# Optimization experiments

Measured on AMD Instinct MI355X. Metric: run time of the kernel, lower is better.

## Reference

```python
import jax, jax.numpy as jnp
import numpy as np

RADIUS = 0.07          # gno_config.gno_radius
SCALES = (1.0, 2.0)    # gno_config.scales


def _kernel_mlp(pair, kW1, kb1, kW2, kb2, kW3, kb3):
    # ChannelMLP inside IntegralTransform: gelu between layers, none after last
    h = jax.nn.gelu(pair @ kW1 + kb1)
    h = jax.nn.gelu(h @ kW2 + kb2)
    return h @ kW3 + kb3


def setup_inputs() -> dict:
    key = jax.random.key(0)
    ks = jax.random.split(key, 8)
    B, N, NL, CD, IN_C, C, H = 2, 2048, 512, 2, 16, 32, 32

    def glorot(k, shape):
        return jax.random.normal(k, shape) / jnp.sqrt(jnp.float32(shape[0]))

    return {
        "x_coord": jax.random.uniform(ks[0], (B, N, CD), dtype=jnp.float32),
        "pndata": jax.random.normal(ks[1], (B, N, IN_C), dtype=jnp.float32),
        "latent_tokens_coord": jax.random.uniform(ks[2], (NL, CD), dtype=jnp.float32),
        # lifting ChannelMLP (n_layers=1 -> single 1x1 conv == linear)
        "W_lift": glorot(ks[3], (IN_C, C)),
        "b_lift": jnp.zeros((C,), jnp.float32),
        # kernel MLP: [2*coord_dim=4] -> 32 -> 32 -> out_channels=32
        "kW1": glorot(ks[4], (2 * CD, H)),
        "kb1": jnp.zeros((H,), jnp.float32),
        "kW2": glorot(ks[5], (H, H)),
        "kb2": jnp.zeros((H,), jnp.float32),
        "kW3": glorot(ks[6], (H, C)),
        "kb3": jnp.zeros((C,), jnp.float32),
    }


def reference(x_coord, pndata, latent_tokens_coord,
              W_lift, b_lift, kW1, kb1, kW2, kb2, kW3, kb3):
    # lifting: [B,N,in_c] -> [B,N,C]
    f = pndata @ W_lift + b_lift

    B, N, CD = x_coord.shape
    NL = latent_tokens_coord.shape[0]

    y = x_coord[:, None, :, :]                      # [B,1,N,CD] source coords
    xq = latent_tokens_coord[None, :, None, :]      # [1,NL,1,CD] query coords
    # kernel input = cat(y_j, x_i) per (query i, source j) pair -> [B,NL,N,2*CD]
    pair = jnp.concatenate([jnp.broadcast_to(y, (B, NL, N, CD)),
                            jnp.broadcast_to(xq, (B, NL, N, CD))], axis=-1)
    kvals = _kernel_mlp(pair, kW1, kb1, kW2, kb2, kW3, kb3)  # [B,NL,N,C]

    d2 = jnp.sum((y - xq) ** 2, axis=-1)            # [B,NL,N] squared distances

    out = jnp.zeros((B, NL, kvals.shape[-1]), f.dtype)
    for s in SCALES:  # fixed small set of scales (2)
        # radius neighbor search expressed as dense mask (faithful to ball query)
        mask = (d2 <= (RADIUS * s) ** 2).astype(f.dtype)      # [B,NL,N]
        cnt = jnp.maximum(jnp.sum(mask, axis=-1), 1.0)        # [B,NL]
        # 'linear' transform: mean_j k(x_i,y_j) * f(y_j) over neighbors
        agg = jnp.einsum('bijc,bjc,bij->bic', kvals, f, mask)
        out = out + agg / cnt[..., None]
    return out  # [B,NL,C]
```

## Files before the change

kernel.cpp:

```cpp
#include <hip/hip_runtime.h>

static constexpr int B_ = 2, N_ = 2048, NL_ = 512, IN_C_ = 16, C_ = 32, H_ = 32;
static constexpr float R1SQ = (float)(0.07 * 0.07);
static constexpr float R2SQ = (float)(0.14 * 0.14);

typedef __attribute__((ext_vector_type(8))) short bf16x8;
typedef __attribute__((ext_vector_type(4))) float f32x4;

__device__ __forceinline__ float gelu_tanh(float x) {
    float z2 = 2.0f * 0.7978845608028654f * x * fmaf(0.044715f * x, x, 1.0f);
    float e = __expf(z2);
    return x * (1.0f - 1.0f / (e + 1.0f));
}

__device__ __forceinline__ short f2bf(float x) {
    unsigned u = __float_as_uint(x);
    u += 0x7fffu + ((u >> 16) & 1u);
    return (short)(u >> 16);
}

__global__ __launch_bounds__(256)
void lift_kernel(const float* __restrict__ pnd,
                 const float* __restrict__ Wl, const float* __restrict__ bl,
                 float* __restrict__ f)
{
    __shared__ float sW[IN_C_ * C_];
    __shared__ float sb[C_];
    int tid = threadIdx.x;
    for (int idx = tid; idx < IN_C_ * C_; idx += 256) sW[idx] = Wl[idx];
    if (tid < C_) sb[tid] = bl[tid];
    __syncthreads();
    int c = tid & 31;
    int row = blockIdx.x * 8 + (tid >> 5);
    if (row >= B_ * N_) return;
    const float* p = pnd + (size_t)row * IN_C_;
    float s = sb[c];
#pragma unroll
    for (int m = 0; m < IN_C_; ++m) s = fmaf(p[m], sW[m * C_ + c], s);
    f[(size_t)row * C_ + c] = s;
}

__global__ __launch_bounds__(128)
void magno_mfma(const float* __restrict__ x_coord,
                const float* __restrict__ lat,
                const float* __restrict__ kW1, const float* __restrict__ kb1,
                const float* __restrict__ kW2, const float* __restrict__ kb2,
                const float* __restrict__ kW3, const float* __restrict__ kb3,
                const float* __restrict__ f,
                float* __restrict__ out)
{
    __shared__ float sR0[H_], sR1[H_], sA1[H_], sB2[H_], sB3[C_];
    __shared__ unsigned jlist[N_];
    __shared__ float strans[2][64 * 33];
    __shared__ float sred[2][C_];
    __shared__ int s_n, s_c1;

    const int tid  = threadIdx.x;
    const int lane = tid & 63;
    const int wid  = tid >> 6;
    const int qd   = lane >> 4;
    const int li   = lane & 15;
    const int bi = blockIdx.x;
    const int b = bi >> 9, i = bi & (NL_ - 1);
    const float xq0 = lat[2 * i], xq1 = lat[2 * i + 1];

    if (tid < H_) {
        sR0[tid] = kW1[tid];
        sR1[tid] = kW1[H_ + tid];
        sA1[tid] = fmaf(xq0, kW1[2 * H_ + tid], fmaf(xq1, kW1[3 * H_ + tid], kb1[tid]));
        sB2[tid] = kb2[tid];
        sB3[tid] = kb3[tid];
    }
    if (tid == 0) { s_n = 0; s_c1 = 0; }

    bf16x8 w2f[2], w3f[2];
#pragma unroll
    for (int nt = 0; nt < 2; ++nt) {
#pragma unroll
        for (int j = 0; j < 8; ++j) {
            int k = qd * 8 + j;
            int n = li + 16 * nt;
            w2f[nt][j] = f2bf(kW2[k * H_ + n]);
            w3f[nt][j] = f2bf(kW3[k * C_ + n]);
        }
    }
    __syncthreads();

    const float2* __restrict__ xc = (const float2*)(x_coord + (size_t)b * N_ * 2);
    for (int j = tid; j < N_; j += 128) {
        float2 y = xc[j];
        float dy0 = y.x - xq0, dy1 = y.y - xq1;
        float d2 = dy0 * dy0 + dy1 * dy1;
        if (d2 <= R2SQ) {
            int pos = atomicAdd(&s_n, 1);
            bool inner = (d2 <= R1SQ);
            jlist[pos] = (unsigned)j | (inner ? 0x80000000u : 0u);
            if (inner) atomicAdd(&s_c1, 1);
        }
    }
    __syncthreads();
    const int n = s_n;
    const float inv2 = 1.0f / (float)(n > 0 ? n : 1);
    const float inv1 = 1.0f / (float)(s_c1 > 0 ? s_c1 : 1);

    float r0v[8], r1v[8], a1v[8], b2v[H_];
#pragma unroll
    for (int j = 0; j < 8; ++j) {
        int k = qd * 8 + j;
        r0v[j] = sR0[k]; r1v[j] = sR1[k]; a1v[j] = sA1[k];
    }
    float* tb = &strans[wid][0];
    const float* fbase = f + (size_t)b * N_ * C_;

    float accA = 0.0f, accB = 0.0f;
    const int nIter = (n + 127) >> 7;

    for (int it = 0; it < nIter; ++it) {
        const int base = it * 128 + 64 * wid;

        bf16x8 hfrag[4];
#pragma unroll
        for (int mt = 0; mt < 4; ++mt) {
            int e = base + 16 * mt + li;
            unsigned pk = jlist[e < N_ ? e : 0];
            int j = (int)(pk & (unsigned)(N_ - 1));
            float2 y = xc[j];
#pragma unroll
            for (int jj = 0; jj < 8; ++jj) {
                float h = gelu_tanh(fmaf(y.x, r0v[jj], fmaf(y.y, r1v[jj], a1v[jj])));
                hfrag[mt][jj] = f2bf(h);
            }
        }

        f32x4 acc2[4][2];
#pragma unroll
        for (int mt = 0; mt < 4; ++mt)
#pragma unroll
            for (int nt = 0; nt < 2; ++nt) {
                f32x4 z = {0.f, 0.f, 0.f, 0.f};
                acc2[mt][nt] = __builtin_amdgcn_mfma_f32_16x16x32_bf16(hfrag[mt], w2f[nt], z, 0, 0, 0);
            }

#pragma unroll
        for (int mt = 0; mt < 4; ++mt)
#pragma unroll
            for (int nt = 0; nt < 2; ++nt)
#pragma unroll
                for (int r = 0; r < 4; ++r) {
                    int nn = li + 16 * nt;
                    float v = gelu_tanh(acc2[mt][nt][r] + sB2[nn]);
                    int el = 16 * mt + qd * 4 + r;
                    tb[el * 33 + nn] = v;
                }
        __syncthreads();

        bf16x8 h2f[4];
#pragma unroll
        for (int mt = 0; mt < 4; ++mt) {
            int row = 16 * mt + li;
#pragma unroll
            for (int jj = 0; jj < 8; ++jj)
                h2f[mt][jj] = f2bf(tb[row * 33 + qd * 8 + jj]);
        }
        __syncthreads();

        f32x4 acc3[4][2];
#pragma unroll
        for (int mt = 0; mt < 4; ++mt)
#pragma unroll
            for (int nt = 0; nt < 2; ++nt) {
                f32x4 z = {0.f, 0.f, 0.f, 0.f};
                acc3[mt][nt] = __builtin_amdgcn_mfma_f32_16x16x32_bf16(h2f[mt], w3f[nt], z, 0, 0, 0);
            }

#pragma unroll
        for (int mt = 0; mt < 4; ++mt)
#pragma unroll
            for (int r = 0; r < 4; ++r) {
                int el = 16 * mt + qd * 4 + r;
                int e = base + el;
                unsigned pk = jlist[e < N_ ? e : 0];
                int j = (int)(pk & (unsigned)(N_ - 1));
                float w = (e < n) ? (inv2 + ((pk & 0x80000000u) ? inv1 : 0.0f)) : 0.0f;
                const float* fr = fbase + (size_t)j * C_;
                float fA = fr[li], fB = fr[li + 16];
                float kvA = acc3[mt][0][r] + sB3[li];
                float kvB = acc3[mt][1][r] + sB3[li + 16];
                accA = fmaf(w * fA, kvA, accA);
                accB = fmaf(w * fB, kvB, accB);
            }
    }

    accA += __shfl_xor(accA, 16, 64);
    accA += __shfl_xor(accA, 32, 64);
    accB += __shfl_xor(accB, 16, 64);
    accB += __shfl_xor(accB, 32, 64);
    if (lane < 16) {
        sred[wid][li] = accA;
        sred[wid][li + 16] = accB;
    }
    __syncthreads();
    if (tid < C_) out[(size_t)bi * C_ + tid] = sred[0][tid] + sred[1][tid];
}

extern "C" void kernel_launch(void* const* d_in, const int* in_sizes, int n_in,
                              void* d_out, int out_size, void* d_ws, size_t ws_size,
                              hipStream_t stream) {
    const float* x_coord = (const float*)d_in[0];
    const float* pndata  = (const float*)d_in[1];
    const float* lat     = (const float*)d_in[2];
    const float* W_lift  = (const float*)d_in[3];
    const float* b_lift  = (const float*)d_in[4];
    const float* kW1     = (const float*)d_in[5];
    const float* kb1     = (const float*)d_in[6];
    const float* kW2     = (const float*)d_in[7];
    const float* kb2     = (const float*)d_in[8];
    const float* kW3     = (const float*)d_in[9];
    const float* kb3     = (const float*)d_in[10];
    float* out = (float*)d_out;

    float* f = (float*)d_ws;
    lift_kernel<<<(B_ * N_ + 7) / 8, 256, 0, stream>>>(pndata, W_lift, b_lift, f);
    magno_mfma<<<B_ * NL_, 128, 0, stream>>>(
        x_coord, lat, kW1, kb1, kW2, kb2, kW3, kb3, f, out);
}
```

Measured before the change: 97.11 us.

## Fuse lifting into main kernel via MFMA, use ballot compaction and bf16 LDS transpose

Removes the separate lift kernel and recomputes the lifted features per gathered neighbor inside the main kernel using an extra bf16 MFMA on the raw input rows. This saves one launch and the workspace write/read of f, but recomputes lifting for every query-neighbor pair and adds bf16 rounding to the lifted features. Neighbor-list compaction now uses wave ballots with one atomic per wave instead of per-element atomics. The layer-2 transpose buffer holds bf16 with padding and is read back as 16-byte vectors, and biases are kept in registers.

```diff
diff --git a/kernel.cpp b/kernel.cpp
--- a/kernel.cpp
+++ b/kernel.cpp
@@ -19,39 +19,20 @@
     return (short)(u >> 16);
 }
 
-__global__ __launch_bounds__(256)
-void lift_kernel(const float* __restrict__ pnd,
-                 const float* __restrict__ Wl, const float* __restrict__ bl,
-                 float* __restrict__ f)
+__global__ __launch_bounds__(128)
+void magno_fused(const float* __restrict__ x_coord,
+                 const float* __restrict__ lat,
+                 const float* __restrict__ kW1, const float* __restrict__ kb1,
+                 const float* __restrict__ kW2, const float* __restrict__ kb2,
+                 const float* __restrict__ kW3, const float* __restrict__ kb3,
+                 const float* __restrict__ pnd,
+                 const float* __restrict__ Wl,
+                 const float* __restrict__ bl,
+                 float* __restrict__ out)
 {
-    __shared__ float sW[IN_C_ * C_];
-    __shared__ float sb[C_];
-    int tid = threadIdx.x;
-    for (int idx = tid; idx < IN_C_ * C_; idx += 256) sW[idx] = Wl[idx];
-    if (tid < C_) sb[tid] = bl[tid];
-    __syncthreads();
-    int c = tid & 31;
-    int row = blockIdx.x * 8 + (tid >> 5);
-    if (row >= B_ * N_) return;
-    const float* p = pnd + (size_t)row * IN_C_;
-    float s = sb[c];
-#pragma unroll
-    for (int m = 0; m < IN_C_; ++m) s = fmaf(p[m], sW[m * C_ + c], s);
-    f[(size_t)row * C_ + c] = s;
-}
-
-__global__ __launch_bounds__(128)
-void magno_mfma(const float* __restrict__ x_coord,
-                const float* __restrict__ lat,
-                const float* __restrict__ kW1, const float* __restrict__ kb1,
-                const float* __restrict__ kW2, const float* __restrict__ kb2,
-                const float* __restrict__ kW3, const float* __restrict__ kb3,
-                const float* __restrict__ f,
-                float* __restrict__ out)
-{
-    __shared__ float sR0[H_], sR1[H_], sA1[H_], sB2[H_], sB3[C_];
+    __shared__ float sR0[H_], sR1[H_], sA1[H_];
     __shared__ unsigned jlist[N_];
-    __shared__ float strans[2][64 * 33];
+    __shared__ __align__(16) short strans[2][64 * 40];
     __shared__ float sred[2][C_];
     __shared__ int s_n, s_c1;
 
@@ -64,38 +45,49 @@
     const int b = bi >> 9, i = bi & (NL_ - 1);
     const float xq0 = lat[2 * i], xq1 = lat[2 * i + 1];
 
+    if (tid == 0) { s_n = 0; s_c1 = 0; }
     if (tid < H_) {
         sR0[tid] = kW1[tid];
         sR1[tid] = kW1[H_ + tid];
         sA1[tid] = fmaf(xq0, kW1[2 * H_ + tid], fmaf(xq1, kW1[3 * H_ + tid], kb1[tid]));
-        sB2[tid] = kb2[tid];
-        sB3[tid] = kb3[tid];
-    }
-    if (tid == 0) { s_n = 0; s_c1 = 0; }
-
-    bf16x8 w2f[2], w3f[2];
+    }
+
+    bf16x8 w2f[2], w3f[2], wlf[2];
 #pragma unroll
     for (int nt = 0; nt < 2; ++nt) {
-#pragma unroll
-        for (int j = 0; j < 8; ++j) {
-            int k = qd * 8 + j;
-            int n = li + 16 * nt;
-            w2f[nt][j] = f2bf(kW2[k * H_ + n]);
-            w3f[nt][j] = f2bf(kW3[k * C_ + n]);
-        }
-    }
+        int n0 = li + 16 * nt;
+#pragma unroll
+        for (int jj = 0; jj < 8; ++jj) {
+            int k = qd * 8 + jj;
+            w2f[nt][jj] = f2bf(kW2[k * H_ + n0]);
+            w3f[nt][jj] = f2bf(kW3[k * C_ + n0]);
+            wlf[nt][jj] = (k < IN_C_) ? f2bf(Wl[k * C_ + n0]) : (short)0;
+        }
+    }
+    const float b2A = kb2[li], b2B = kb2[li + 16];
+    const float b3A = kb3[li], b3B = kb3[li + 16];
+    const float blA = bl[li],  blB = bl[li + 16];
     __syncthreads();
 
     const float2* __restrict__ xc = (const float2*)(x_coord + (size_t)b * N_ * 2);
-    for (int j = tid; j < N_; j += 128) {
-        float2 y = xc[j];
+    const unsigned long long ltmask = (1ull << lane) - 1ull;
+    for (int j0 = tid; j0 < N_; j0 += 128) {
+        float2 y = xc[j0];
         float dy0 = y.x - xq0, dy1 = y.y - xq1;
         float d2 = dy0 * dy0 + dy1 * dy1;
-        if (d2 <= R2SQ) {
-            int pos = atomicAdd(&s_n, 1);
-            bool inner = (d2 <= R1SQ);
-            jlist[pos] = (unsigned)j | (inner ? 0x80000000u : 0u);
-            if (inner) atomicAdd(&s_c1, 1);
+        bool in2 = d2 <= R2SQ;
+        bool in1 = d2 <= R1SQ;
+        unsigned long long m2 = __ballot(in2);
+        unsigned long long m1 = __ballot(in1);
+        int basew = 0;
+        if (lane == 0) {
+            basew = atomicAdd(&s_n, __popcll(m2));
+            atomicAdd(&s_c1, __popcll(m1));
+        }
+        basew = __shfl(basew, 0, 64);
+        if (in2) {
+            int pos = basew + __popcll(m2 & ltmask);
+            jlist[pos] = (unsigned)j0 | (in1 ? 0x80000000u : 0u);
         }
     }
     __syncthreads();
@@ -103,14 +95,15 @@
     const float inv2 = 1.0f / (float)(n > 0 ? n : 1);
     const float inv1 = 1.0f / (float)(s_c1 > 0 ? s_c1 : 1);
 
-    float r0v[8], r1v[8], a1v[8], b2v[H_];
-#pragma unroll
-    for (int j = 0; j < 8; ++j) {
-        int k = qd * 8 + j;
-        r0v[j] = sR0[k]; r1v[j] = sR1[k]; a1v[j] = sA1[k];
-    }
-    float* tb = &strans[wid][0];
-    const float* fbase = f + (size_t)b * N_ * C_;
+    float r0v[8], r1v[8], a1v[8];
+#pragma unroll
+    for (int jj = 0; jj < 8; ++jj) {
+        int k = qd * 8 + jj;
+        r0v[jj] = sR0[k]; r1v[jj] = sR1[k]; a1v[jj] = sA1[k];
+    }
+
+    const float* __restrict__ pbase = pnd + (size_t)b * N_ * IN_C_;
+    short* tb = &strans[wid][0];
 
     float accA = 0.0f, accB = 0.0f;
     const int nIter = (n + 127) >> 7;
@@ -118,7 +111,7 @@
     for (int it = 0; it < nIter; ++it) {
         const int base = it * 128 + 64 * wid;
 
-        bf16x8 hfrag[4];
+        bf16x8 hfrag[4], paf[4];
 #pragma unroll
         for (int mt = 0; mt < 4; ++mt) {
             int e = base + 16 * mt + li;
@@ -126,42 +119,49 @@
             int j = (int)(pk & (unsigned)(N_ - 1));
             float2 y = xc[j];
 #pragma unroll
-            for (int jj = 0; jj < 8; ++jj) {
-                float h = gelu_tanh(fmaf(y.x, r0v[jj], fmaf(y.y, r1v[jj], a1v[jj])));
-                hfrag[mt][jj] = f2bf(h);
-            }
-        }
-
-        f32x4 acc2[4][2];
+            for (int jj = 0; jj < 8; ++jj)
+                hfrag[mt][jj] = f2bf(gelu_tanh(fmaf(y.x, r0v[jj], fmaf(y.y, r1v[jj], a1v[jj]))));
+            if (qd < 2) {
+                const float4* p4 = (const float4*)(pbase + (size_t)j * IN_C_ + qd * 8);
+                float4 v0 = p4[0], v1 = p4[1];
+                paf[mt][0] = f2bf(v0.x); paf[mt][1] = f2bf(v0.y);
+                paf[mt][2] = f2bf(v0.z); paf[mt][3] = f2bf(v0.w);
+                paf[mt][4] = f2bf(v1.x); paf[mt][5] = f2bf(v1.y);
+                paf[mt][6] = f2bf(v1.z); paf[mt][7] = f2bf(v1.w);
+            } else {
+#pragma unroll
+                for (int jj = 0; jj < 8; ++jj) paf[mt][jj] = (short)0;
+            }
+        }
+
+        f32x4 accF[4][2], acc2[4][2];
 #pragma unroll
         for (int mt = 0; mt < 4; ++mt)
 #pragma unroll
             for (int nt = 0; nt < 2; ++nt) {
                 f32x4 z = {0.f, 0.f, 0.f, 0.f};
+                accF[mt][nt] = __builtin_amdgcn_mfma_f32_16x16x32_bf16(paf[mt],   wlf[nt], z, 0, 0, 0);
                 acc2[mt][nt] = __builtin_amdgcn_mfma_f32_16x16x32_bf16(hfrag[mt], w2f[nt], z, 0, 0, 0);
             }
 
 #pragma unroll
         for (int mt = 0; mt < 4; ++mt)
 #pragma unroll
-            for (int nt = 0; nt < 2; ++nt)
+            for (int nt = 0; nt < 2; ++nt) {
+                float bb = nt ? b2B : b2A;
+                int hid = li + 16 * nt;
 #pragma unroll
                 for (int r = 0; r < 4; ++r) {
-                    int nn = li + 16 * nt;
-                    float v = gelu_tanh(acc2[mt][nt][r] + sB2[nn]);
-                    int el = 16 * mt + qd * 4 + r;
-                    tb[el * 33 + nn] = v;
+                    int entry = 16 * mt + 4 * qd + r;
+                    tb[entry * 40 + hid] = f2bf(gelu_tanh(acc2[mt][nt][r] + bb));
                 }
+            }
         __syncthreads();
 
         bf16x8 h2f[4];
 #pragma unroll
-        for (int mt = 0; mt < 4; ++mt) {
-            int row = 16 * mt + li;
-#pragma unroll
-            for (int jj = 0; jj < 8; ++jj)
-                h2f[mt][jj] = f2bf(tb[row * 33 + qd * 8 + jj]);
-        }
+        for (int mt = 0; mt < 4; ++mt)
+            h2f[mt] = *(const bf16x8*)&tb[(li + 16 * mt) * 40 + qd * 8];
         __syncthreads();
 
         f32x4 acc3[4][2];
@@ -177,17 +177,13 @@
         for (int mt = 0; mt < 4; ++mt)
 #pragma unroll
             for (int r = 0; r < 4; ++r) {
-                int el = 16 * mt + qd * 4 + r;
-                int e = base + el;
+                int e = base + 16 * mt + 4 * qd + r;
                 unsigned pk = jlist[e < N_ ? e : 0];
-                int j = (int)(pk & (unsigned)(N_ - 1));
                 float w = (e < n) ? (inv2 + ((pk & 0x80000000u) ? inv1 : 0.0f)) : 0.0f;
-                const float* fr = fbase + (size_t)j * C_;
-                float fA = fr[li], fB = fr[li + 16];
-                float kvA = acc3[mt][0][r] + sB3[li];
-                float kvB = acc3[mt][1][r] + sB3[li + 16];
-                accA = fmaf(w * fA, kvA, accA);
-                accB = fmaf(w * fB, kvB, accB);
+                float fA = accF[mt][0][r] + blA;
+                float fB = accF[mt][1][r] + blB;
+                accA = fmaf(w * fA, acc3[mt][0][r] + b3A, accA);
+                accB = fmaf(w * fB, acc3[mt][1][r] + b3B, accB);
             }
     }
 
@@ -219,8 +215,7 @@
     const float* kb3     = (const float*)d_in[10];
     float* out = (float*)d_out;
 
-    float* f = (float*)d_ws;
-    lift_kernel<<<(B_ * N_ + 7) / 8, 256, 0, stream>>>(pndata, W_lift, b_lift, f);
-    magno_mfma<<<B_ * NL_, 128, 0, stream>>>(
-        x_coord, lat, kW1, kb1, kW2, kb2, kW3, kb3, f, out);
-}
+    magno_fused<<<B_ * NL_, 128, 0, stream>>>(
+        x_coord, lat, kW1, kb1, kW2, kb2, kW3, kb3,
+        pndata, W_lift, b_lift, out);
+}
```

Result: slower. 101.4 us (+4.4%).
